# Performance work log

Measured on AMD Instinct MI355X. Metric: run time of the kernel, lower is better.

## Reference

```python
import jax, jax.numpy as jnp
import numpy as np

NUM_HEADS = 8
WINDOW = 7
DILATION = 1
EPS = 1e-5


def channel_ln(x, w, b):
    # x: [B, C, H, W]; normalize over channel dim (axis=1)
    mu = jnp.mean(x, axis=1, keepdims=True)
    var = jnp.var(x, axis=1, keepdims=True)
    xhat = (x - mu) * jax.lax.rsqrt(var + EPS)
    return xhat * w[None, :, None, None] + b[None, :, None, None]


def local_mask(H, W, window, dilation):
    r = (window // 2) * dilation
    ii, jj = jnp.meshgrid(jnp.arange(H), jnp.arange(W), indexing="ij")
    ii = ii.reshape(-1)
    jj = jj.reshape(-1)
    di = jnp.abs(ii[:, None] - ii[None, :])
    dj = jnp.abs(jj[:, None] - jj[None, :])
    m = (di <= r) & (dj <= r)
    if dilation > 1:
        m = m & (di % dilation == 0) & (dj % dilation == 0)
    return m  # [N, N] bool


def local_attention(x, qkv_w, qkv_b, proj_w, proj_b):
    B, C, H, W = x.shape
    N = H * W
    hd = C // NUM_HEADS
    t = x.reshape(B, C, N).transpose(0, 2, 1)            # [B, N, C]
    qkv = t @ qkv_w.T + qkv_b                            # [B, N, 3C]
    qkv = qkv.reshape(B, N, 3, NUM_HEADS, hd)
    q, k, v = (qkv[:, :, i].transpose(0, 2, 1, 3) for i in range(3))  # [B,h,N,d]
    scale = 1.0 / jnp.sqrt(jnp.asarray(hd, x.dtype))
    scores = jnp.einsum("bhnd,bhmd->bhnm", q, k) * scale  # [B,h,N,N]
    mask = local_mask(H, W, WINDOW, DILATION)             # [N,N]
    scores = jnp.where(mask[None, None], scores, jnp.asarray(-jnp.inf, x.dtype))
    attn = jax.nn.softmax(scores, axis=-1)
    out = jnp.einsum("bhnm,bhmd->bhnd", attn, v)          # [B,h,N,d]
    out = out.transpose(0, 2, 1, 3).reshape(B, N, C)      # [B,N,C]
    out = out @ proj_w.T + proj_b
    return out.transpose(0, 2, 1).reshape(B, C, H, W)


def mlp2d(x, fc1_w, fc1_b, fc2_w, fc2_b):
    # 1x1 convs == per-pixel linear over channels
    h = jnp.einsum("bchw,oc->bohw", x, fc1_w) + fc1_b[None, :, None, None]
    h = jax.nn.gelu(h, approximate=False)
    return jnp.einsum("bchw,oc->bohw", h, fc2_w) + fc2_b[None, :, None, None]


def setup_inputs() -> dict:
    key = jax.random.key(0)
    ks = jax.random.split(key, 12)
    B, C, H, W = 1, 256, 56, 56
    hidden = 4 * C
    s = lambda fan: 1.0 / np.sqrt(fan)
    return {
        "x": jax.random.normal(ks[0], (B, C, H, W), jnp.float32),
        "norm1_w": jnp.ones((C,), jnp.float32),
        "norm1_b": jnp.zeros((C,), jnp.float32),
        "qkv_w": jax.random.normal(ks[1], (3 * C, C), jnp.float32) * s(C),
        "qkv_b": jnp.zeros((3 * C,), jnp.float32),
        "proj_w": jax.random.normal(ks[2], (C, C), jnp.float32) * s(C),
        "proj_b": jnp.zeros((C,), jnp.float32),
        "norm2_w": jnp.ones((C,), jnp.float32),
        "norm2_b": jnp.zeros((C,), jnp.float32),
        "fc1_w": jax.random.normal(ks[3], (hidden, C), jnp.float32) * s(C),
        "fc1_b": jnp.zeros((hidden,), jnp.float32),
        "fc2_w": jax.random.normal(ks[4], (C, hidden), jnp.float32) * s(hidden),
        "fc2_b": jnp.zeros((C,), jnp.float32),
    }


def reference(x, norm1_w, norm1_b, qkv_w, qkv_b, proj_w, proj_b,
              norm2_w, norm2_b, fc1_w, fc1_b, fc2_w, fc2_b):
    x = x + local_attention(channel_ln(x, norm1_w, norm1_b), qkv_w, qkv_b, proj_w, proj_b)
    x = x + mlp2d(channel_ln(x, norm2_w, norm2_b), fc1_w, fc1_b, fc2_w, fc2_b)
    return x
```

## Files before the change

### kernel.cpp

```cpp
#include <hip/hip_runtime.h>
#include <math.h>


typedef unsigned int uint;
typedef unsigned short ushort;
typedef unsigned long long u64;
typedef __attribute__((ext_vector_type(8))) short short8;
typedef __attribute__((ext_vector_type(4))) float floatx4;
typedef __attribute__((ext_vector_type(4))) unsigned short ushort4v;

#define AS1(p) (const __attribute__((address_space(1))) void*)(p)
#define AS3(p) (__attribute__((address_space(3))) void*)(p)

__device__ __forceinline__ float bf2f(ushort u) {
  union { uint i; float f; } v; v.i = ((uint)u) << 16; return v.f;
}
__device__ __forceinline__ ushort f2bf(float f) {
  union { float f; uint i; } v; v.f = f;
  uint u = v.i;
  return (ushort)((u + 0x7fffu + ((u >> 16) & 1u)) >> 16);
}

__device__ __forceinline__ void stage64(const ushort* src, int kstride,
                                        ushort* dstBase, int tid) {
  const int srow = tid >> 5;
  const int scb  = (tid & 31) ^ srow;
  const ushort* g = src + (size_t)srow * kstride + scb * 8;
  ushort* d = dstBase + tid * 8;
  #pragma unroll
  for (int r = 0; r < 8; ++r) {
    __builtin_amdgcn_global_load_lds(AS1(g), AS3(d), 16, 0, 0);
    g += 8 * kstride;
    d += 2048;
  }
}

__device__ __forceinline__ void compute64(const ushort* As, const ushort* Bs,
                                          int w, int lane, floatx4 acc[4]) {
  const int fm = lane & 15;
  const int q  = lane >> 4;
  const int swz = fm & 7;
  const int arow = (w * 16 + fm) * 256;
  #pragma unroll
  for (int kt = 0; kt < 8; ++kt) {
    const int blk = ((kt * 4 + q) ^ swz) * 8;
    short8 af = *(const short8*)&As[arow + blk];
    #pragma unroll
    for (int nt = 0; nt < 4; ++nt) {
      short8 bfr = *(const short8*)&Bs[(nt * 16 + fm) * 256 + blk];
      acc[nt] = __builtin_amdgcn_mfma_f32_16x16x32_bf16(af, bfr, acc[nt], 0, 0, 0);
    }
  }
}

__global__ __launch_bounds__(256) void prep_kernel(
    const float* __restrict__ x, const float* __restrict__ n1w,
    const float* __restrict__ n1b, const float* __restrict__ qkvw,
    ushort* __restrict__ t1, ushort* __restrict__ wcat)
{
  const int tid = threadIdx.x;
  const int bid = blockIdx.x;
  if (bid >= 196) {
    int idx = (bid - 196) * 256 + tid;
    wcat[idx] = f2bf(qkvw[idx]);
    return;
  }
  __shared__ float tile[256 * 17];
  __shared__ float red[2][16][16];
  __shared__ float mu[16], rsv[16];
  const int n0 = bid * 16;
  const int px = tid & 15, grp = tid >> 4;
  #pragma unroll 4
  for (int it = 0; it < 16; ++it) {
    int c = it * 16 + grp;
    tile[c * 17 + px] = x[(size_t)c * 3136 + n0 + px];
  }
  __syncthreads();
  float s = 0.f, ss = 0.f;
  #pragma unroll
  for (int i = 0; i < 16; ++i) {
    float v = tile[(grp * 16 + i) * 17 + px];
    s += v; ss += v * v;
  }
  red[0][px][grp] = s; red[1][px][grp] = ss;
  __syncthreads();
  if (tid < 16) {
    float s2 = 0.f, ss2 = 0.f;
    #pragma unroll
    for (int g = 0; g < 16; ++g) { s2 += red[0][tid][g]; ss2 += red[1][tid][g]; }
    float m = s2 * (1.f / 256.f);
    float var = ss2 * (1.f / 256.f) - m * m;
    mu[tid] = m;
    rsv[tid] = rsqrtf(var + 1e-5f);
  }
  __syncthreads();
  const float wc = n1w[tid], bc = n1b[tid];
  #pragma unroll 4
  for (int p = 0; p < 16; ++p) {
    float v = tile[tid * 17 + p];
    t1[(size_t)(n0 + p) * 256 + tid] = f2bf((v - mu[p]) * rsv[p] * wc + bc);
  }
}

__global__ __launch_bounds__(256, 2) void qkv_kernel(
    const ushort* __restrict__ A, const ushort* __restrict__ B,
    const float* __restrict__ bias, ushort* __restrict__ out,
    const float* __restrict__ projw, const float* __restrict__ f1w,
    const float* __restrict__ f2w, ushort* __restrict__ wcat)
{
  const int tid = threadIdx.x;
  if (blockIdx.y >= 49) {
    int c = (blockIdx.y - 49) * 12 + blockIdx.x;
    int idx = c * 256 + tid;
    float v;
    if (idx < 65536)        v = projw[idx];
    else if (idx < 327680)  v = f1w[idx - 65536];
    else                    v = f2w[idx - 327680];
    wcat[196608 + idx] = f2bf(v);
    return;
  }
  __shared__ ushort As[16384], Bs[16384];
  const int lane = tid & 63, w = tid >> 6;
  const int m0 = blockIdx.y * 64, n0 = blockIdx.x * 64;
  floatx4 acc[4] = {{0.f,0.f,0.f,0.f},{0.f,0.f,0.f,0.f},
                    {0.f,0.f,0.f,0.f},{0.f,0.f,0.f,0.f}};
  stage64(A + (size_t)m0 * 256, 256, As, tid);
  stage64(B + (size_t)n0 * 256, 256, Bs, tid);
  asm volatile("s_waitcnt vmcnt(0)" ::: "memory");
  __syncthreads();
  compute64(As, Bs, w, lane, acc);
  const int fm = lane & 15, q4 = (lane >> 4) * 4;
  #pragma unroll
  for (int nt = 0; nt < 4; ++nt)
    #pragma unroll
    for (int r = 0; r < 4; ++r) {
      int m = m0 + w * 16 + q4 + r;
      int n = n0 + nt * 16 + fm;
      float v = acc[nt][r] + bias[n];
      if (n < 256) v *= 0.17677669529663687f;
      out[(size_t)m * 768 + n] = f2bf(v);
    }
}

#define AM_SMEM 145952

__global__ __launch_bounds__(512, 1) void attnmlp_kernel(
    const ushort* __restrict__ qkv, const ushort* __restrict__ pw_bf,
    const float* __restrict__ projb, const float* __restrict__ x,
    const ushort* __restrict__ f1_bf, const float* __restrict__ f1b,
    const ushort* __restrict__ f2_bf, const float* __restrict__ f2b,
    const float* __restrict__ n2w, const float* __restrict__ n2b,
    float* __restrict__ outf)
{
  __shared__ __align__(16) char smem[AM_SMEM];
  ushort* Kh    = (ushort*)smem;
  ushort* Vh    = (ushort*)(smem + 52000);
  float*  pr    = (float*)(smem + 103200);
  ushort* aas   = (ushort*)(smem + 137504);
  ushort* pslab = (ushort*)smem;
  float*  x1s   = (float*)(smem + 103200);
  ushort* hbuf  = (ushort*)smem;
  ushort* fslab = (ushort*)(smem + 32768);
  ushort* t2s   = (ushort*)(smem + 120096);
  float*  pstat = (float*)(smem + 128288);
  float*  stats = (float*)(smem + 129312);

  const int tid = threadIdx.x;
  const int wv = tid >> 6, lane = tid & 63;
  const int fm = lane & 15, q = lane >> 4;
  const int l4 = lane >> 2, lb = lane & 3;
  const int i0 = (blockIdx.x / 14) * 4, j0 = (blockIdx.x % 14) * 4;

  for (int s = tid; s < 3200; s += 512) {
    int p = s >> 5, ck = s & 31;
    int ii = i0 - 3 + p / 10, jj = j0 - 3 + p % 10;
    if (ii >= 0 && ii < 56 && jj >= 0 && jj < 56) {
      const ushort* kr = qkv + (size_t)(ii * 56 + jj) * 768 + 256 + ck * 8;
      short8 kv = *(const short8*)kr;
      u64 lo = ((const u64*)&kv)[0], hi = ((const u64*)&kv)[1];
      *(u64*)&Kh[p * 260 + ck * 8] = lo;
      *(u64*)&Kh[p * 260 + ck * 8 + 4] = hi;
      *(short8*)&Vh[p * 256 + ck * 8] = *(const short8*)(kr + 256);
    } else {
      *(u64*)&Kh[p * 260 + ck * 8] = 0ull;
      *(u64*)&Kh[p * 260 + ck * 8 + 4] = 0ull;
      short8 z = {0, 0, 0, 0, 0, 0, 0, 0};
      *(short8*)&Vh[p * 256 + ck * 8] = z;
    }
  }
  __syncthreads();

  {
    const int h = lane >> 3, mg = lane & 7;
    #pragma unroll
    for (int qq = 0; qq < 2; ++qq) {
      const int p = wv * 2 + qq;
      const int qi = p >> 2, qj = p & 3;
      const int iq = i0 + qi, jq = j0 + qj;
      const ushort* qp = qkv + (size_t)(iq * 56 + jq) * 768 + h * 32;
      float qf[32];
      #pragma unroll
      for (int u = 0; u < 4; ++u) {
        short8 qv = *(const short8*)(qp + u * 8);
        #pragma unroll
        for (int e = 0; e < 8; ++e) qf[u * 8 + e] = bf2f((ushort)qv[e]);
      }
      float sv[7];
      float mx = -1e30f;
      #pragma unroll
      for (int k = 0; k < 7; ++k) {
        int m = mg + 8 * k;
        float s = -1e30f;
        if (m < 49) {
          int mi = m / 7, mj = m % 7;
          int ii = iq + mi - 3, jj = jq + mj - 3;
          if (ii >= 0 && ii < 56 && jj >= 0 && jj < 56) {
            int hrow = (qi + mi) * 10 + (qj + mj);
            const u64* k8 = (const u64*)&Kh[hrow * 260 + h * 32];
            float a = 0.f;
            #pragma unroll
            for (int u = 0; u < 8; ++u) {
              u64 kv = k8[u];
              #pragma unroll
              for (int e = 0; e < 4; ++e)
                a += qf[u * 4 + e] * bf2f((ushort)(kv >> (16 * e)));
            }
            s = a;
          }
        }
        sv[k] = s;
        mx = fmaxf(mx, s);
      }
      mx = fmaxf(mx, __shfl_xor(mx, 1));
      mx = fmaxf(mx, __shfl_xor(mx, 2));
      mx = fmaxf(mx, __shfl_xor(mx, 4));
      float sm = 0.f;
      #pragma unroll
      for (int k = 0; k < 7; ++k) { sv[k] = __expf(sv[k] - mx); sm += sv[k]; }
      sm += __shfl_xor(sm, 1);
      sm += __shfl_xor(sm, 2);
      sm += __shfl_xor(sm, 4);
      float inv = 1.f / sm;
      #pragma unroll
      for (int k = 0; k < 7; ++k) {
        int m = mg + 8 * k;
        pr[(p * 8 + h) * 67 + m] = sv[k] * inv;
      }
    }
  }
  __syncthreads();

  ushort* ps0 = pslab + wv * 2048;
  ushort* ps1 = ps0 + 1024;
#define STAGE_P(kt, buf) do { \
    _Pragma("unroll") \
    for (int i_ = 0; i_ < 2; ++i_) { \
      int row_ = i_ * 16 + l4; \
      const ushort* g_ = pw_bf + (size_t)(wv * 32 + row_) * 256 + (kt) * 32 + (lb ^ (row_ & 3)) * 8; \
      __builtin_amdgcn_global_load_lds(AS1(g_), AS3((buf) + i_ * 512 + lane * 8), 16, 0, 0); \
    } } while (0)
  STAGE_P(0, ps0);

  {
    const int p = tid >> 5, cg = tid & 31, hh = cg >> 2;
    const int qi = p >> 2, qj = p & 3;
    float acc8[8] = {0, 0, 0, 0, 0, 0, 0, 0};
    #pragma unroll
    for (int mi = 0; mi < 7; ++mi)
      #pragma unroll
      for (int mj = 0; mj < 7; ++mj) {
        int m = mi * 7 + mj;
        int hrow = (qi + mi) * 10 + (qj + mj);
        float pm = pr[(p * 8 + hh) * 67 + m];
        short8 v8 = *(const short8*)&Vh[hrow * 256 + cg * 8];
        #pragma unroll
        for (int e = 0; e < 8; ++e)
          acc8[e] += pm * bf2f((ushort)v8[e]);
      }
    short8 o;
    #pragma unroll
    for (int e = 0; e < 8; ++e) o[e] = (short)f2bf(acc8[e]);
    *(short8*)&aas[p * 264 + cg * 8] = o;
  }
  __syncthreads();

  {
    floatx4 pacc[2] = {{0.f,0.f,0.f,0.f},{0.f,0.f,0.f,0.f}};
    for (int kt = 0; kt < 8; ++kt) {
      ushort* cur = (kt & 1) ? ps1 : ps0;
      ushort* nxt = (kt & 1) ? ps0 : ps1;
      if (kt < 7) {
        STAGE_P(kt + 1, nxt);
        asm volatile("s_waitcnt vmcnt(2)" ::: "memory");
      } else {
        asm volatile("s_waitcnt vmcnt(0)" ::: "memory");
      }
      short8 af = *(const short8*)&aas[fm * 264 + kt * 32 + q * 8];
      #pragma unroll
      for (int nt = 0; nt < 2; ++nt) {
        int r = nt * 16 + fm;
        short8 bfr = *(const short8*)&cur[r * 32 + (q ^ (r & 3)) * 8];
        pacc[nt] = __builtin_amdgcn_mfma_f32_16x16x32_bf16(af, bfr, pacc[nt], 0, 0, 0);
      }
    }
    #pragma unroll
    for (int nt = 0; nt < 2; ++nt) {
      int ch = wv * 32 + nt * 16 + fm;
      floatx4 rx = *(const floatx4*)(x + (size_t)ch * 3136 + (i0 + q) * 56 + j0);
      #pragma unroll
      for (int r = 0; r < 4; ++r) {
        int px = q * 4 + r;
        x1s[px * 264 + ch] = pacc[nt][r] + projb[ch] + rx[r];
      }
    }
  }
  ushort* fs0 = fslab + wv * 4096;
  ushort* fs1 = fs0 + 2048;
#define STAGE_F1(c, kt, buf) do { \
    _Pragma("unroll") \
    for (int i_ = 0; i_ < 4; ++i_) { \
      int row_ = i_ * 16 + l4; \
      const ushort* g_ = f1_bf + (size_t)((c) * 64 + row_) * 256 + (kt) * 32 + (lb ^ (row_ & 3)) * 8; \
      __builtin_amdgcn_global_load_lds(AS1(g_), AS3((buf) + i_ * 512 + lane * 8), 16, 0, 0); \
    } } while (0)
  STAGE_F1(wv, 0, fs0);
  __syncthreads();

  floatx4 xv[2];
  xv[0] = *(const floatx4*)&x1s[fm * 264 + wv * 32 + q * 4];
  xv[1] = *(const floatx4*)&x1s[fm * 264 + wv * 32 + 16 + q * 4];
  {
    float s = 0.f, ss = 0.f;
    #pragma unroll
    for (int nt = 0; nt < 2; ++nt)
      #pragma unroll
      for (int e = 0; e < 4; ++e) { s += xv[nt][e]; ss += xv[nt][e] * xv[nt][e]; }
    s += __shfl_xor(s, 16); ss += __shfl_xor(ss, 16);
    s += __shfl_xor(s, 32); ss += __shfl_xor(ss, 32);
    if (lane < 16) { pstat[(wv * 16 + lane) * 2] = s; pstat[(wv * 16 + lane) * 2 + 1] = ss; }
  }
  __syncthreads();
  if (tid < 16) {
    float s2 = 0.f, ss2 = 0.f;
    #pragma unroll
    for (int ww = 0; ww < 8; ++ww) {
      s2 += pstat[(ww * 16 + tid) * 2];
      ss2 += pstat[(ww * 16 + tid) * 2 + 1];
    }
    float mu = s2 * (1.f / 256.f);
    float var = ss2 * (1.f / 256.f) - mu * mu;
    stats[tid * 2] = mu;
    stats[tid * 2 + 1] = rsqrtf(var + 1e-5f);
  }
  __syncthreads();
  {
    float mu = stats[fm * 2], rs = stats[fm * 2 + 1];
    #pragma unroll
    for (int nt = 0; nt < 2; ++nt) {
      int ch0 = wv * 32 + nt * 16 + q * 4;
      ushort4v o;
      #pragma unroll
      for (int e = 0; e < 4; ++e)
        o[e] = f2bf((xv[nt][e] - mu) * rs * n2w[ch0 + e] + n2b[ch0 + e]);
      int slot = ch0 >> 3;
      *(ushort4v*)&t2s[fm * 256 + ((slot ^ (fm & 7)) * 8) + (ch0 & 7)] = o;
    }
  }
  float f1br[2][4];
  #pragma unroll
  for (int ci = 0; ci < 2; ++ci)
    #pragma unroll
    for (int nt = 0; nt < 4; ++nt)
      f1br[ci][nt] = f1b[(wv + ci * 8) * 64 + nt * 16 + fm];
  __syncthreads();

  {
    floatx4 fa[4] = {{0.f,0.f,0.f,0.f},{0.f,0.f,0.f,0.f},
                     {0.f,0.f,0.f,0.f},{0.f,0.f,0.f,0.f}};
    for (int sidx = 0; sidx < 16; ++sidx) {
      const int kt = sidx & 7;
      const int ci = sidx >> 3;
      ushort* cur = (sidx & 1) ? fs1 : fs0;
      ushort* nxt = (sidx & 1) ? fs0 : fs1;
      if (sidx < 15) {
        int s1 = sidx + 1;
        STAGE_F1(wv + (s1 >> 3) * 8, s1 & 7, nxt);
        asm volatile("s_waitcnt vmcnt(4)" ::: "memory");
      } else {
        asm volatile("s_waitcnt vmcnt(0)" ::: "memory");
      }
      short8 af = *(const short8*)&t2s[fm * 256 + (((kt * 4 + q) ^ (fm & 7)) * 8)];
      #pragma unroll
      for (int nt = 0; nt < 4; ++nt) {
        int r = nt * 16 + fm;
        short8 bfr = *(const short8*)&cur[r * 32 + (q ^ (r & 3)) * 8];
        fa[nt] = __builtin_amdgcn_mfma_f32_16x16x32_bf16(af, bfr, fa[nt], 0, 0, 0);
      }
      if (kt == 7) {
        #pragma unroll
        for (int nt = 0; nt < 4; ++nt) {
          int hc = (wv + ci * 8) * 64 + nt * 16 + fm;
          #pragma unroll
          for (int r4 = 0; r4 < 4; ++r4) {
            int prow = q * 4 + r4;
            float v = fa[nt][r4] + f1br[ci][nt];
            v = 0.5f * v * (1.0f + erff(v * 0.70710678118654752f));
            hbuf[prow * 1024 + (((hc >> 3) ^ (prow & 7)) * 8) + (hc & 7)] = f2bf(v);
            fa[nt][r4] = 0.f;
          }
        }
      }
    }
  }
  ushort* gs0 = fs0;
  ushort* gs1 = fs0 + 1024;
#define STAGE_F2(kt, buf) do { \
    _Pragma("unroll") \
    for (int i_ = 0; i_ < 2; ++i_) { \
      int row_ = i_ * 16 + l4; \
      const ushort* g_ = f2_bf + (size_t)(wv * 32 + row_) * 1024 + (kt) * 32 + (lb ^ (row_ & 3)) * 8; \
      __builtin_amdgcn_global_load_lds(AS1(g_), AS3((buf) + i_ * 512 + lane * 8), 16, 0, 0); \
    } } while (0)
  STAGE_F2(0, gs0);
  __syncthreads();

  {
    floatx4 ga[2] = {{0.f,0.f,0.f,0.f},{0.f,0.f,0.f,0.f}};
    for (int kt = 0; kt < 32; ++kt) {
      ushort* cur = (kt & 1) ? gs1 : gs0;
      ushort* nxt = (kt & 1) ? gs0 : gs1;
      if (kt < 31) {
        STAGE_F2(kt + 1, nxt);
        asm volatile("s_waitcnt vmcnt(2)" ::: "memory");
      } else {
        asm volatile("s_waitcnt vmcnt(0)" ::: "memory");
      }
      short8 bfr = *(const short8*)&hbuf[fm * 1024 + (((kt * 4 + q) ^ (fm & 7)) * 8)];
      #pragma unroll
      for (int mt = 0; mt < 2; ++mt) {
        int r = mt * 16 + fm;
        short8 af = *(const short8*)&cur[r * 32 + (q ^ (r & 3)) * 8];
        ga[mt] = __builtin_amdgcn_mfma_f32_16x16x32_bf16(af, bfr, ga[mt], 0, 0, 0);
      }
    }
    #pragma unroll
    for (int mt = 0; mt < 2; ++mt) {
      #pragma unroll
      for (int r4 = 0; r4 < 4; ++r4) {
        int ch = wv * 32 + mt * 16 + q * 4 + r4;
        int n = (i0 + (fm >> 2)) * 56 + j0 + (fm & 3);
        outf[(size_t)ch * 3136 + n] = ga[mt][r4] + f2b[ch] + xv[mt][r4];
      }
    }
  }
#undef STAGE_P
#undef STAGE_F1
#undef STAGE_F2
}

extern "C" void kernel_launch(void* const* d_in, const int* in_sizes, int n_in,
                              void* d_out, int out_size, void* d_ws, size_t ws_size,
                              hipStream_t stream) {
  const float* x     = (const float*)d_in[0];
  const float* n1w   = (const float*)d_in[1];
  const float* n1b   = (const float*)d_in[2];
  const float* qkvw  = (const float*)d_in[3];
  const float* qkvb  = (const float*)d_in[4];
  const float* projw = (const float*)d_in[5];
  const float* projb = (const float*)d_in[6];
  const float* n2w   = (const float*)d_in[7];
  const float* n2b   = (const float*)d_in[8];
  const float* f1w   = (const float*)d_in[9];
  const float* f1b   = (const float*)d_in[10];
  const float* f2w   = (const float*)d_in[11];
  const float* f2b   = (const float*)d_in[12];

  char* ws = (char*)d_ws;
  ushort* wcat = (ushort*)(ws + 0);
  ushort* t    = (ushort*)(ws + 4784128);
  ushort* qh   = (ushort*)(ws + 6389760);

  const ushort* qw_bf = wcat;
  const ushort* pw_bf = wcat + 196608;
  const ushort* f1_bf = wcat + 262144;
  const ushort* f2_bf = wcat + 524288;
  float* outf = (float*)d_out;

  hipLaunchKernelGGL(prep_kernel, dim3(964), dim3(256), 0, stream,
                     x, n1w, n1b, qkvw, t, wcat);
  hipLaunchKernelGGL(qkv_kernel, dim3(12, 241), dim3(256), 0, stream,
                     t, qw_bf, qkvb, qh, projw, f1w, f2w, wcat);
  hipLaunchKernelGGL(attnmlp_kernel, dim3(196), dim3(512), 0, stream,
                     qh, pw_bf, projb, x, f1_bf, f1b, f2_bf, f2b,
                     n2w, n2b, outf);
}
```

Measured before the change: 125.9 us.

## Fuse channel LayerNorm and QKV weight conversion into the QKV GEMM kernel

```diff
diff --git a/kernel.cpp b/kernel.cpp
--- a/kernel.cpp
+++ b/kernel.cpp
@@ -19,20 +19,6 @@
   union { float f; uint i; } v; v.f = f;
   uint u = v.i;
   return (ushort)((u + 0x7fffu + ((u >> 16) & 1u)) >> 16);
-}
-
-__device__ __forceinline__ void stage64(const ushort* src, int kstride,
-                                        ushort* dstBase, int tid) {
-  const int srow = tid >> 5;
-  const int scb  = (tid & 31) ^ srow;
-  const ushort* g = src + (size_t)srow * kstride + scb * 8;
-  ushort* d = dstBase + tid * 8;
-  #pragma unroll
-  for (int r = 0; r < 8; ++r) {
-    __builtin_amdgcn_global_load_lds(AS1(g), AS3(d), 16, 0, 0);
-    g += 8 * kstride;
-    d += 2048;
-  }
 }
 
 __device__ __forceinline__ void compute64(const ushort* As, const ushort* Bs,
@@ -53,57 +39,9 @@
   }
 }
 
-__global__ __launch_bounds__(256) void prep_kernel(
+__global__ __launch_bounds__(256, 2) void qkv_kernel(
     const float* __restrict__ x, const float* __restrict__ n1w,
     const float* __restrict__ n1b, const float* __restrict__ qkvw,
-    ushort* __restrict__ t1, ushort* __restrict__ wcat)
-{
-  const int tid = threadIdx.x;
-  const int bid = blockIdx.x;
-  if (bid >= 196) {
-    int idx = (bid - 196) * 256 + tid;
-    wcat[idx] = f2bf(qkvw[idx]);
-    return;
-  }
-  __shared__ float tile[256 * 17];
-  __shared__ float red[2][16][16];
-  __shared__ float mu[16], rsv[16];
-  const int n0 = bid * 16;
-  const int px = tid & 15, grp = tid >> 4;
-  #pragma unroll 4
-  for (int it = 0; it < 16; ++it) {
-    int c = it * 16 + grp;
-    tile[c * 17 + px] = x[(size_t)c * 3136 + n0 + px];
-  }
-  __syncthreads();
-  float s = 0.f, ss = 0.f;
-  #pragma unroll
-  for (int i = 0; i < 16; ++i) {
-    float v = tile[(grp * 16 + i) * 17 + px];
-    s += v; ss += v * v;
-  }
-  red[0][px][grp] = s; red[1][px][grp] = ss;
-  __syncthreads();
-  if (tid < 16) {
-    float s2 = 0.f, ss2 = 0.f;
-    #pragma unroll
-    for (int g = 0; g < 16; ++g) { s2 += red[0][tid][g]; ss2 += red[1][tid][g]; }
-    float m = s2 * (1.f / 256.f);
-    float var = ss2 * (1.f / 256.f) - m * m;
-    mu[tid] = m;
-    rsv[tid] = rsqrtf(var + 1e-5f);
-  }
-  __syncthreads();
-  const float wc = n1w[tid], bc = n1b[tid];
-  #pragma unroll 4
-  for (int p = 0; p < 16; ++p) {
-    float v = tile[tid * 17 + p];
-    t1[(size_t)(n0 + p) * 256 + tid] = f2bf((v - mu[p]) * rsv[p] * wc + bc);
-  }
-}
-
-__global__ __launch_bounds__(256, 2) void qkv_kernel(
-    const ushort* __restrict__ A, const ushort* __restrict__ B,
     const float* __restrict__ bias, ushort* __restrict__ out,
     const float* __restrict__ projw, const float* __restrict__ f1w,
     const float* __restrict__ f2w, ushort* __restrict__ wcat)
@@ -120,14 +58,64 @@
     return;
   }
   __shared__ ushort As[16384], Bs[16384];
+  __shared__ float psum[4][64], psumsq[4][64];
   const int lane = tid & 63, w = tid >> 6;
   const int m0 = blockIdx.y * 64, n0 = blockIdx.x * 64;
+
+  float arr[64];
+  {
+    const float* xp = x + (size_t)(w * 64) * 3136 + m0 + lane;
+    float s = 0.f, ss = 0.f;
+    #pragma unroll
+    for (int i = 0; i < 64; ++i) {
+      float v = xp[(size_t)i * 3136];
+      arr[i] = v;
+      s += v; ss += v * v;
+    }
+    psum[w][lane] = s;
+    psumsq[w][lane] = ss;
+  }
+
+  #pragma unroll
+  for (int k = 0; k < 8; ++k) {
+    int srow = k * 8 + (tid >> 5);
+    int cb = tid & 31;
+    int gb = cb ^ (srow & 7);
+    const float* gp = qkvw + (size_t)(n0 + srow) * 256 + gb * 8;
+    floatx4 a = *(const floatx4*)gp;
+    floatx4 b = *(const floatx4*)(gp + 4);
+    short8 o;
+    #pragma unroll
+    for (int e = 0; e < 4; ++e) {
+      o[e]     = (short)f2bf(a[e]);
+      o[e + 4] = (short)f2bf(b[e]);
+    }
+    *(short8*)&Bs[srow * 256 + cb * 8] = o;
+  }
+  __syncthreads();
+
+  {
+    float s  = psum[0][lane] + psum[1][lane] + psum[2][lane] + psum[3][lane];
+    float ss = psumsq[0][lane] + psumsq[1][lane] + psumsq[2][lane] + psumsq[3][lane];
+    float mu = s * (1.f / 256.f);
+    float var = ss * (1.f / 256.f) - mu * mu;
+    float rsv = rsqrtf(var + 1e-5f);
+    #pragma unroll
+    for (int g = 0; g < 8; ++g) {
+      short8 o;
+      #pragma unroll
+      for (int e = 0; e < 8; ++e) {
+        int ch = w * 64 + g * 8 + e;
+        o[e] = (short)f2bf((arr[g * 8 + e] - mu) * rsv * n1w[ch] + n1b[ch]);
+      }
+      int gblk = w * 8 + g;
+      *(short8*)&As[lane * 256 + ((gblk ^ (lane & 7)) * 8)] = o;
+    }
+  }
+  __syncthreads();
+
   floatx4 acc[4] = {{0.f,0.f,0.f,0.f},{0.f,0.f,0.f,0.f},
                     {0.f,0.f,0.f,0.f},{0.f,0.f,0.f,0.f}};
-  stage64(A + (size_t)m0 * 256, 256, As, tid);
-  stage64(B + (size_t)n0 * 256, 256, Bs, tid);
-  asm volatile("s_waitcnt vmcnt(0)" ::: "memory");
-  __syncthreads();
   compute64(As, Bs, w, lane, acc);
   const int fm = lane & 15, q4 = (lane >> 4) * 4;
   #pragma unroll
@@ -477,19 +465,15 @@
 
   char* ws = (char*)d_ws;
   ushort* wcat = (ushort*)(ws + 0);
-  ushort* t    = (ushort*)(ws + 4784128);
   ushort* qh   = (ushort*)(ws + 6389760);
 
-  const ushort* qw_bf = wcat;
   const ushort* pw_bf = wcat + 196608;
   const ushort* f1_bf = wcat + 262144;
   const ushort* f2_bf = wcat + 524288;
   float* outf = (float*)d_out;
 
-  hipLaunchKernelGGL(prep_kernel, dim3(964), dim3(256), 0, stream,
-                     x, n1w, n1b, qkvw, t, wcat);
   hipLaunchKernelGGL(qkv_kernel, dim3(12, 241), dim3(256), 0, stream,
-                     t, qw_bf, qkvb, qh, projw, f1w, f2w, wcat);
+                     x, n1w, n1b, qkvw, qkvb, qh, projw, f1w, f2w, wcat);
   hipLaunchKernelGGL(attnmlp_kernel, dim3(196), dim3(512), 0, stream,
                      qh, pw_bf, projb, x, f1_bf, f1b, f2_bf, f2b,
                      n2w, n2b, outf);
```

New measurement: 128.5 us. 1.02x slower.

## Deepen weight-staging pipelines with per-wave LDS ring buffers in fused attn-MLP kernel

Applied to the files above, without the earlier changes.

```diff
diff --git a/kernel.cpp b/kernel.cpp
--- a/kernel.cpp
+++ b/kernel.cpp
@@ -142,7 +142,7 @@
     }
 }
 
-#define AM_SMEM 145952
+#define AM_SMEM 147104
 
 __global__ __launch_bounds__(512, 1) void attnmlp_kernel(
     const ushort* __restrict__ qkv, const ushort* __restrict__ pw_bf,
@@ -155,21 +155,27 @@
   __shared__ __align__(16) char smem[AM_SMEM];
   ushort* Kh    = (ushort*)smem;
   ushort* Vh    = (ushort*)(smem + 52000);
+  ushort* rings = (ushort*)smem;
   float*  pr    = (float*)(smem + 103200);
+  float*  x1s   = (float*)(smem + 103200);
+  ushort* hbuf  = (ushort*)(smem + 103200);
   ushort* aas   = (ushort*)(smem + 137504);
-  ushort* pslab = (ushort*)smem;
-  float*  x1s   = (float*)(smem + 103200);
-  ushort* hbuf  = (ushort*)smem;
-  ushort* fslab = (ushort*)(smem + 32768);
-  ushort* t2s   = (ushort*)(smem + 120096);
-  float*  pstat = (float*)(smem + 128288);
-  float*  stats = (float*)(smem + 129312);
+  ushort* t2s   = (ushort*)(smem + 137504);
+  float*  pstat = (float*)(smem + 145952);
+  float*  stats = (float*)(smem + 146976);
 
   const int tid = threadIdx.x;
   const int wv = tid >> 6, lane = tid & 63;
   const int fm = lane & 15, q = lane >> 4;
   const int l4 = lane >> 2, lb = lane & 3;
   const int i0 = (blockIdx.x / 14) * 4, j0 = (blockIdx.x % 14) * 4;
+
+  ushort* prb[3];
+  #pragma unroll
+  for (int i = 0; i < 3; ++i) prb[i] = rings + wv * 3072 + i * 1024;
+  ushort* rb[6];
+  #pragma unroll
+  for (int i = 0; i < 6; ++i) rb[i] = rings + wv * 6144 + i * 1024;
 
   for (int s = tid; s < 3200; s += 512) {
     int p = s >> 5, ck = s & 31;
@@ -250,8 +256,6 @@
   }
   __syncthreads();
 
-  ushort* ps0 = pslab + wv * 2048;
-  ushort* ps1 = ps0 + 1024;
 #define STAGE_P(kt, buf) do { \
     _Pragma("unroll") \
     for (int i_ = 0; i_ < 2; ++i_) { \
@@ -259,7 +263,8 @@
       const ushort* g_ = pw_bf + (size_t)(wv * 32 + row_) * 256 + (kt) * 32 + (lb ^ (row_ & 3)) * 8; \
       __builtin_amdgcn_global_load_lds(AS1(g_), AS3((buf) + i_ * 512 + lane * 8), 16, 0, 0); \
     } } while (0)
-  STAGE_P(0, ps0);
+  STAGE_P(0, prb[0]);
+  STAGE_P(1, prb[1]);
 
   {
     const int p = tid >> 5, cg = tid & 31, hh = cg >> 2;
@@ -286,15 +291,15 @@
 
   {
     floatx4 pacc[2] = {{0.f,0.f,0.f,0.f},{0.f,0.f,0.f,0.f}};
+    #pragma unroll
     for (int kt = 0; kt < 8; ++kt) {
-      ushort* cur = (kt & 1) ? ps1 : ps0;
-      ushort* nxt = (kt & 1) ? ps0 : ps1;
-      if (kt < 7) {
-        STAGE_P(kt + 1, nxt);
-        asm volatile("s_waitcnt vmcnt(2)" ::: "memory");
-      } else {
+      if (kt < 6) {
+        STAGE_P(kt + 2, prb[(kt + 2) % 3]);
+        asm volatile("s_waitcnt vmcnt(4)" ::: "memory");
+      } else if (kt == 6) {
         asm volatile("s_waitcnt vmcnt(0)" ::: "memory");
       }
+      ushort* cur = prb[kt % 3];
       short8 af = *(const short8*)&aas[fm * 264 + kt * 32 + q * 8];
       #pragma unroll
       for (int nt = 0; nt < 2; ++nt) {
@@ -314,17 +319,17 @@
       }
     }
   }
-  ushort* fs0 = fslab + wv * 4096;
-  ushort* fs1 = fs0 + 2048;
+  __syncthreads();
+
 #define STAGE_F1(c, kt, buf) do { \
     _Pragma("unroll") \
-    for (int i_ = 0; i_ < 4; ++i_) { \
+    for (int i_ = 0; i_ < 2; ++i_) { \
       int row_ = i_ * 16 + l4; \
-      const ushort* g_ = f1_bf + (size_t)((c) * 64 + row_) * 256 + (kt) * 32 + (lb ^ (row_ & 3)) * 8; \
+      const ushort* g_ = f1_bf + (size_t)((c) * 32 + row_) * 256 + (kt) * 32 + (lb ^ (row_ & 3)) * 8; \
       __builtin_amdgcn_global_load_lds(AS1(g_), AS3((buf) + i_ * 512 + lane * 8), 16, 0, 0); \
     } } while (0)
-  STAGE_F1(wv, 0, fs0);
-  __syncthreads();
+  #pragma unroll
+  for (int s = 0; s < 5; ++s) STAGE_F1(wv, s, rb[s]);
 
   floatx4 xv[2];
   xv[0] = *(const floatx4*)&x1s[fm * 264 + wv * 32 + q * 4];
@@ -366,40 +371,38 @@
       *(ushort4v*)&t2s[fm * 256 + ((slot ^ (fm & 7)) * 8) + (ch0 & 7)] = o;
     }
   }
-  float f1br[2][4];
-  #pragma unroll
-  for (int ci = 0; ci < 2; ++ci)
-    #pragma unroll
-    for (int nt = 0; nt < 4; ++nt)
-      f1br[ci][nt] = f1b[(wv + ci * 8) * 64 + nt * 16 + fm];
-  __syncthreads();
-
-  {
-    floatx4 fa[4] = {{0.f,0.f,0.f,0.f},{0.f,0.f,0.f,0.f},
-                     {0.f,0.f,0.f,0.f},{0.f,0.f,0.f,0.f}};
-    for (int sidx = 0; sidx < 16; ++sidx) {
+  float f1br[4][2];
+  #pragma unroll
+  for (int ci = 0; ci < 4; ++ci)
+    #pragma unroll
+    for (int nt = 0; nt < 2; ++nt)
+      f1br[ci][nt] = f1b[(wv + ci * 8) * 32 + nt * 16 + fm];
+  __syncthreads();
+
+  {
+    floatx4 fa[2] = {{0.f,0.f,0.f,0.f},{0.f,0.f,0.f,0.f}};
+    for (int sidx = 0; sidx < 32; ++sidx) {
+      if (sidx < 27) {
+        int s5 = sidx + 5;
+        STAGE_F1((s5 >> 3) * 8 + wv, s5 & 7, rb[s5 % 6]);
+        asm volatile("s_waitcnt vmcnt(10)" ::: "memory");
+      } else if (sidx == 27) {
+        asm volatile("s_waitcnt vmcnt(0)" ::: "memory");
+      }
       const int kt = sidx & 7;
-      const int ci = sidx >> 3;
-      ushort* cur = (sidx & 1) ? fs1 : fs0;
-      ushort* nxt = (sidx & 1) ? fs0 : fs1;
-      if (sidx < 15) {
-        int s1 = sidx + 1;
-        STAGE_F1(wv + (s1 >> 3) * 8, s1 & 7, nxt);
-        asm volatile("s_waitcnt vmcnt(4)" ::: "memory");
-      } else {
-        asm volatile("s_waitcnt vmcnt(0)" ::: "memory");
-      }
+      ushort* cur = rb[sidx % 6];
       short8 af = *(const short8*)&t2s[fm * 256 + (((kt * 4 + q) ^ (fm & 7)) * 8)];
       #pragma unroll
-      for (int nt = 0; nt < 4; ++nt) {
+      for (int nt = 0; nt < 2; ++nt) {
         int r = nt * 16 + fm;
         short8 bfr = *(const short8*)&cur[r * 32 + (q ^ (r & 3)) * 8];
         fa[nt] = __builtin_amdgcn_mfma_f32_16x16x32_bf16(af, bfr, fa[nt], 0, 0, 0);
       }
       if (kt == 7) {
+        const int ci = sidx >> 3;
         #pragma unroll
-        for (int nt = 0; nt < 4; ++nt) {
-          int hc = (wv + ci * 8) * 64 + nt * 16 + fm;
+        for (int nt = 0; nt < 2; ++nt) {
+          int hc = (wv + ci * 8) * 32 + nt * 16 + fm;
           #pragma unroll
           for (int r4 = 0; r4 < 4; ++r4) {
             int prow = q * 4 + r4;
@@ -412,8 +415,6 @@
       }
     }
   }
-  ushort* gs0 = fs0;
-  ushort* gs1 = fs0 + 1024;
 #define STAGE_F2(kt, buf) do { \
     _Pragma("unroll") \
     for (int i_ = 0; i_ < 2; ++i_) { \
@@ -421,20 +422,20 @@
       const ushort* g_ = f2_bf + (size_t)(wv * 32 + row_) * 1024 + (kt) * 32 + (lb ^ (row_ & 3)) * 8; \
       __builtin_amdgcn_global_load_lds(AS1(g_), AS3((buf) + i_ * 512 + lane * 8), 16, 0, 0); \
     } } while (0)
-  STAGE_F2(0, gs0);
+  #pragma unroll
+  for (int s = 0; s < 5; ++s) STAGE_F2(s, rb[s]);
   __syncthreads();
 
   {
     floatx4 ga[2] = {{0.f,0.f,0.f,0.f},{0.f,0.f,0.f,0.f}};
     for (int kt = 0; kt < 32; ++kt) {
-      ushort* cur = (kt & 1) ? gs1 : gs0;
-      ushort* nxt = (kt & 1) ? gs0 : gs1;
-      if (kt < 31) {
-        STAGE_F2(kt + 1, nxt);
-        asm volatile("s_waitcnt vmcnt(2)" ::: "memory");
-      } else {
+      if (kt < 27) {
+        STAGE_F2(kt + 5, rb[(kt + 5) % 6]);
+        asm volatile("s_waitcnt vmcnt(10)" ::: "memory");
+      } else if (kt == 27) {
         asm volatile("s_waitcnt vmcnt(0)" ::: "memory");
       }
+      ushort* cur = rb[kt % 6];
       short8 bfr = *(const short8*)&hbuf[fm * 1024 + (((kt * 4 + q) ^ (fm & 7)) * 8)];
       #pragma unroll
       for (int mt = 0; mt < 2; ++mt) {
```

Result: slower. 134.0 us (+6.4%).
